# Kernel optimization log

Hardware: AMD Instinct MI355X
Metric: run time of the kernel (lower is better)

The kernel has to match this reference:

```python
import jax, jax.numpy as jnp
import numpy as np

T = 32            # timesteps_count
DT = 1e-3
TAU_MEM_INV = 100.0   # norse LIFParameters default (1/1e-2)
TAU_SYN_INV = 200.0   # norse default (1/5e-3)
V_TH = 1.0
ALPHA = 100.0         # SuperSpike surrogate slope


@jax.custom_vjp
def superspike(x):
    # Heaviside forward, SuperSpike surrogate backward (norse 'super' method)
    return (x > 0).astype(x.dtype)

def _ss_fwd(x):
    return (x > 0).astype(x.dtype), x

def _ss_bwd(x, g):
    return (g / (ALPHA * jnp.abs(x) + 1.0) ** 2,)

superspike.defvjp(_ss_fwd, _ss_bwd)


def setup_inputs() -> dict:
    key = jax.random.key(0)
    k1, k2 = jax.random.split(key)
    image = jax.random.uniform(k1, (4096, 1, 28, 28), dtype=jnp.float32)
    # LILinearCell input weights, shape [out_features, in_features]
    W = jax.random.normal(k2, (10, 784), dtype=jnp.float32) * np.sqrt(2.0 / 784.0).astype(np.float32)
    return {"image": image, "W": W}


def reference(image, W):
    B = image.shape[0]
    x = image.reshape(B, -1)  # [B, 784] constant input current

    def step(carry, _):
        v_enc, v0, i0, v_out, i_out = carry
        # --- ConstantCurrentLIFEncoder (lif_current_encoder step) ---
        v_enc = v_enc + DT * TAU_MEM_INV * (-v_enc + x)
        z_enc = superspike(v_enc - V_TH)
        v_enc = v_enc - z_enc * v_enc  # reset to v_reset = 0
        # --- LIFCell (feed-forward LIF step) ---
        v_dec = v0 + DT * TAU_MEM_INV * (-v0 + i0)
        i_dec = i0 - DT * TAU_SYN_INV * i0
        z0 = superspike(v_dec - V_TH)
        v0_new = (1.0 - z0) * v_dec          # v_reset = 0
        i0_new = i_dec + z_enc
        # --- LILinearCell (leaky integrator with linear input) ---
        i_jump = i_out + z0 @ W.T            # [B, 10]
        v_out_new = v_out + DT * TAU_MEM_INV * (-v_out + i_jump)
        i_out_new = i_jump - DT * TAU_SYN_INV * i_jump
        return (v_enc, v0_new, i0_new, v_out_new, i_out_new), v_out_new

    z784 = jnp.zeros_like(x)
    z10 = jnp.zeros((B, 10), dtype=x.dtype)
    _, vs = jax.lax.scan(step, (z784, z784, z784, z10, z10), None, length=T)
    v_max = jnp.max(vs, axis=0)              # max over timesteps, [B, 10]
    return jax.nn.log_softmax(v_max, axis=1)
```

## Files before the change

### kernel.cpp

```cpp
#include <hip/hip_runtime.h>
#include <math.h>


#define T_STEPS 32
#define N_IN 784
#define N_OUT 10
#define NK 4

__global__ __launch_bounds__(256) void snn_fused_kernel(
    const float* __restrict__ image,
    const float* __restrict__ W,
    float* __restrict__ out)
{
    constexpr float DT_TMI  = 0.1f;
    constexpr float DEC_SYN = 0.8f;
    constexpr float V_TH    = 1.0f;
    constexpr float NEG_LOG10 = -2.30258509299404568402f;

    const int b   = blockIdx.x;
    const int tid = threadIdx.x;
    const float* __restrict__ x_row = image + (size_t)b * N_IN;

    float xk[NK];
    int   jn[NK];
    int   can_spike = 0;
#pragma unroll
    for (int k = 0; k < NK; ++k) {
        int j = tid + 256 * k;
        jn[k] = j;
        xk[k] = (j < N_IN) ? x_row[j] : 0.0f;
        can_spike |= (xk[k] > V_TH);
    }

    if (!__syncthreads_or(can_spike)) {
        if (tid < N_OUT) out[(size_t)b * N_OUT + tid] = NEG_LOG10;
        return;
    }

    float v_enc[NK], v0[NK], i0[NK];
#pragma unroll
    for (int k = 0; k < NK; ++k) { v_enc[k] = 0.0f; v0[k] = 0.0f; i0[k] = 0.0f; }

    __shared__ float red[4][N_OUT];
    __shared__ float s_vout[N_OUT], s_iout[N_OUT], s_vmax[N_OUT];
    if (tid < N_OUT) {
        s_vout[tid] = 0.0f;
        s_iout[tid] = 0.0f;
        s_vmax[tid] = -INFINITY;
    }

    for (int t = 0; t < T_STEPS; ++t) {
        float s[N_OUT];
#pragma unroll
        for (int o = 0; o < N_OUT; ++o) s[o] = 0.0f;
        int any_spike = 0;

#pragma unroll
        for (int k = 0; k < NK; ++k) {
            v_enc[k] += DT_TMI * (xk[k] - v_enc[k]);
            float z_enc = (v_enc[k] > V_TH) ? 1.0f : 0.0f;
            v_enc[k] = (v_enc[k] > V_TH) ? 0.0f : v_enc[k];
            float v_dec = v0[k] + DT_TMI * (i0[k] - v0[k]);
            float i_dec = DEC_SYN * i0[k];
            bool  z0    = v_dec > V_TH;
            v0[k] = z0 ? 0.0f : v_dec;
            i0[k] = i_dec + z_enc;
            if (z0 && jn[k] < N_IN) {
                any_spike = 1;
#pragma unroll
                for (int o = 0; o < N_OUT; ++o)
                    s[o] += W[o * N_IN + jn[k]];
            }
        }

        const int any = __syncthreads_or(any_spike);

        if (any) {
#pragma unroll
            for (int o = 0; o < N_OUT; ++o) {
                float v = s[o];
                v += __shfl_down(v, 32, 64);
                v += __shfl_down(v, 16, 64);
                v += __shfl_down(v,  8, 64);
                v += __shfl_down(v,  4, 64);
                v += __shfl_down(v,  2, 64);
                v += __shfl_down(v,  1, 64);
                s[o] = v;
            }
            const int wave = tid >> 6;
            if ((tid & 63) == 0) {
#pragma unroll
                for (int o = 0; o < N_OUT; ++o) red[wave][o] = s[o];
            }
            __syncthreads();
        }

        if (tid < N_OUT) {
            float jump = s_iout[tid];
            if (any)
                jump += red[0][tid] + red[1][tid] + red[2][tid] + red[3][tid];
            float v = s_vout[tid] + DT_TMI * (jump - s_vout[tid]);
            s_vout[tid] = v;
            s_iout[tid] = DEC_SYN * jump;
            s_vmax[tid] = fmaxf(s_vmax[tid], v);
        }
    }

    __syncthreads();
    if (tid == 0) {
        float m = -INFINITY;
#pragma unroll
        for (int o = 0; o < N_OUT; ++o) m = fmaxf(m, s_vmax[o]);
        float sum = 0.0f;
#pragma unroll
        for (int o = 0; o < N_OUT; ++o) sum += expf(s_vmax[o] - m);
        const float lse = m + logf(sum);
        float* orow = out + (size_t)b * N_OUT;
#pragma unroll
        for (int o = 0; o < N_OUT; ++o) orow[o] = s_vmax[o] - lse;
    }
}

extern "C" void kernel_launch(void* const* d_in, const int* in_sizes, int n_in,
                              void* d_out, int out_size, void* d_ws, size_t ws_size,
                              hipStream_t stream) {
    const float* image = (const float*)d_in[0];
    const float* W     = (const float*)d_in[1];
    float*       out   = (float*)d_out;

    const int B = in_sizes[0] / N_IN;
    snn_fused_kernel<<<B, 256, 0, stream>>>(image, W, out);
}
```

Measured before the change: 62.43 us.

## Map one image row per wavefront and keep neuron state in global workspace

```diff
diff --git a/kernel.cpp b/kernel.cpp
--- a/kernel.cpp
+++ b/kernel.cpp
@@ -2,122 +2,137 @@
 #include <math.h>
 
 
+#define N_IN   784
+#define N_OUT  10
 #define T_STEPS 32
-#define N_IN 784
-#define N_OUT 10
-#define NK 4
+#define ROW_F4 196
+#define WS_ROW 2382
 
-__global__ __launch_bounds__(256) void snn_fused_kernel(
+__global__ __launch_bounds__(256) void snn_wave_kernel(
     const float* __restrict__ image,
     const float* __restrict__ W,
-    float* __restrict__ out)
+    float* __restrict__ out,
+    float* __restrict__ ws,
+    int B)
 {
     constexpr float DT_TMI  = 0.1f;
     constexpr float DEC_SYN = 0.8f;
     constexpr float V_TH    = 1.0f;
     constexpr float NEG_LOG10 = -2.30258509299404568402f;
 
-    const int b   = blockIdx.x;
-    const int tid = threadIdx.x;
-    const float* __restrict__ x_row = image + (size_t)b * N_IN;
+    const int wave = threadIdx.x >> 6;
+    const int lane = threadIdx.x & 63;
+    const int row  = blockIdx.x * 4 + wave;
+    if (row >= B) return;
 
-    float xk[NK];
-    int   jn[NK];
-    int   can_spike = 0;
-#pragma unroll
-    for (int k = 0; k < NK; ++k) {
-        int j = tid + 256 * k;
-        jn[k] = j;
-        xk[k] = (j < N_IN) ? x_row[j] : 0.0f;
-        can_spike |= (xk[k] > V_TH);
-    }
+    const float4* __restrict__ x4 = (const float4*)(image + (size_t)row * N_IN);
 
-    if (!__syncthreads_or(can_spike)) {
-        if (tid < N_OUT) out[(size_t)b * N_OUT + tid] = NEG_LOG10;
+    const bool has4 = (lane < 4);
+    float4 c0 = x4[lane];
+    float4 c1 = x4[lane + 64];
+    float4 c2 = x4[lane + 128];
+    float4 c3 = has4 ? x4[lane + 192] : make_float4(0.f, 0.f, 0.f, 0.f);
+
+    float m = fmaxf(fmaxf(fmaxf(c0.x, c0.y), fmaxf(c0.z, c0.w)),
+                    fmaxf(fmaxf(c1.x, c1.y), fmaxf(c1.z, c1.w)));
+    m = fmaxf(m, fmaxf(fmaxf(c2.x, c2.y), fmaxf(c2.z, c2.w)));
+    m = fmaxf(m, fmaxf(fmaxf(c3.x, c3.y), fmaxf(c3.z, c3.w)));
+
+    if (!__any(m > V_TH)) {
+        if (lane < N_OUT) out[(size_t)row * N_OUT + lane] = NEG_LOG10;
         return;
     }
 
-    float v_enc[NK], v0[NK], i0[NK];
+    float* const rb   = ws + (size_t)row * WS_ROW;
+    float* const p_ve = rb;
+    float* const p_v0 = rb + N_IN;
+    float* const p_i0 = rb + 2 * N_IN;
+    float* const p_ro = rb + 3 * N_IN;
+
+    const float xv[16] = { c0.x, c0.y, c0.z, c0.w,  c1.x, c1.y, c1.z, c1.w,
+                           c2.x, c2.y, c2.z, c2.w,  c3.x, c3.y, c3.z, c3.w };
+    const int   cbase[4] = { lane, lane + 64, lane + 128, lane + 192 };
+    const int   nch = has4 ? 4 : 3;
+
+    for (int c = 0; c < nch; ++c) {
+        const int j0 = 4 * cbase[c];
 #pragma unroll
-    for (int k = 0; k < NK; ++k) { v_enc[k] = 0.0f; v0[k] = 0.0f; i0[k] = 0.0f; }
-
-    __shared__ float red[4][N_OUT];
-    __shared__ float s_vout[N_OUT], s_iout[N_OUT], s_vmax[N_OUT];
-    if (tid < N_OUT) {
-        s_vout[tid] = 0.0f;
-        s_iout[tid] = 0.0f;
-        s_vmax[tid] = -INFINITY;
+        for (int e = 0; e < 4; ++e) {
+            p_ve[j0 + e] = 0.0f; p_v0[j0 + e] = 0.0f; p_i0[j0 + e] = 0.0f;
+        }
+    }
+    if (lane == 0) {
+#pragma unroll
+        for (int o = 0; o < N_OUT; ++o) {
+            p_ro[o] = 0.0f;
+            p_ro[10 + o] = 0.0f;
+            p_ro[20 + o] = -INFINITY;
+        }
     }
 
     for (int t = 0; t < T_STEPS; ++t) {
         float s[N_OUT];
 #pragma unroll
         for (int o = 0; o < N_OUT; ++o) s[o] = 0.0f;
-        int any_spike = 0;
 
+        for (int c = 0; c < nch; ++c) {
+            const int j0 = 4 * cbase[c];
 #pragma unroll
-        for (int k = 0; k < NK; ++k) {
-            v_enc[k] += DT_TMI * (xk[k] - v_enc[k]);
-            float z_enc = (v_enc[k] > V_TH) ? 1.0f : 0.0f;
-            v_enc[k] = (v_enc[k] > V_TH) ? 0.0f : v_enc[k];
-            float v_dec = v0[k] + DT_TMI * (i0[k] - v0[k]);
-            float i_dec = DEC_SYN * i0[k];
-            bool  z0    = v_dec > V_TH;
-            v0[k] = z0 ? 0.0f : v_dec;
-            i0[k] = i_dec + z_enc;
-            if (z0 && jn[k] < N_IN) {
-                any_spike = 1;
+            for (int e = 0; e < 4; ++e) {
+                const int j = j0 + e;
+                const float x = xv[4 * c + e];
+                float ve = p_ve[j], v0 = p_v0[j], i0 = p_i0[j];
+                ve += DT_TMI * (x - ve);
+                const float z_enc = (ve > V_TH) ? 1.0f : 0.0f;
+                ve = (ve > V_TH) ? 0.0f : ve;
+                const float v_dec = v0 + DT_TMI * (i0 - v0);
+                const float i_dec = DEC_SYN * i0;
+                const bool  z0    = v_dec > V_TH;
+                p_ve[j] = ve;
+                p_v0[j] = z0 ? 0.0f : v_dec;
+                p_i0[j] = i_dec + z_enc;
+                if (z0) {
 #pragma unroll
-                for (int o = 0; o < N_OUT; ++o)
-                    s[o] += W[o * N_IN + jn[k]];
+                    for (int o = 0; o < N_OUT; ++o) s[o] += W[o * N_IN + j];
+                }
             }
         }
 
-        const int any = __syncthreads_or(any_spike);
+#pragma unroll
+        for (int o = 0; o < N_OUT; ++o) {
+            float v = s[o];
+            v += __shfl_down(v, 32, 64);
+            v += __shfl_down(v, 16, 64);
+            v += __shfl_down(v,  8, 64);
+            v += __shfl_down(v,  4, 64);
+            v += __shfl_down(v,  2, 64);
+            v += __shfl_down(v,  1, 64);
+            s[o] = v;
+        }
 
-        if (any) {
+        if (lane == 0) {
 #pragma unroll
             for (int o = 0; o < N_OUT; ++o) {
-                float v = s[o];
-                v += __shfl_down(v, 32, 64);
-                v += __shfl_down(v, 16, 64);
-                v += __shfl_down(v,  8, 64);
-                v += __shfl_down(v,  4, 64);
-                v += __shfl_down(v,  2, 64);
-                v += __shfl_down(v,  1, 64);
-                s[o] = v;
+                const float jump = p_ro[10 + o] + s[o];
+                const float v    = p_ro[o] + DT_TMI * (jump - p_ro[o]);
+                p_ro[o]      = v;
+                p_ro[10 + o] = DEC_SYN * jump;
+                p_ro[20 + o] = fmaxf(p_ro[20 + o], v);
             }
-            const int wave = tid >> 6;
-            if ((tid & 63) == 0) {
-#pragma unroll
-                for (int o = 0; o < N_OUT; ++o) red[wave][o] = s[o];
-            }
-            __syncthreads();
-        }
-
-        if (tid < N_OUT) {
-            float jump = s_iout[tid];
-            if (any)
-                jump += red[0][tid] + red[1][tid] + red[2][tid] + red[3][tid];
-            float v = s_vout[tid] + DT_TMI * (jump - s_vout[tid]);
-            s_vout[tid] = v;
-            s_iout[tid] = DEC_SYN * jump;
-            s_vmax[tid] = fmaxf(s_vmax[tid], v);
         }
     }
 
-    __syncthreads();
-    if (tid == 0) {
-        float m = -INFINITY;
+    if (lane == 0) {
+        float mm = -INFINITY;
 #pragma unroll
-        for (int o = 0; o < N_OUT; ++o) m = fmaxf(m, s_vmax[o]);
+        for (int o = 0; o < N_OUT; ++o) mm = fmaxf(mm, p_ro[20 + o]);
         float sum = 0.0f;
 #pragma unroll
-        for (int o = 0; o < N_OUT; ++o) sum += expf(s_vmax[o] - m);
-        const float lse = m + logf(sum);
-        float* orow = out + (size_t)b * N_OUT;
+        for (int o = 0; o < N_OUT; ++o) sum += expf(p_ro[20 + o] - mm);
+        const float lse = mm + logf(sum);
+        float* orow = out + (size_t)row * N_OUT;
 #pragma unroll
-        for (int o = 0; o < N_OUT; ++o) orow[o] = s_vmax[o] - lse;
+        for (int o = 0; o < N_OUT; ++o) orow[o] = p_ro[20 + o] - lse;
     }
 }
 
@@ -129,5 +144,6 @@
     float*       out   = (float*)d_out;
 
     const int B = in_sizes[0] / N_IN;
-    snn_fused_kernel<<<B, 256, 0, stream>>>(image, W, out);
+    const int blocks = (B + 3) / 4;
+    snn_wave_kernel<<<blocks, 256, 0, stream>>>(image, W, out, (float*)d_ws, B);
 }
```

After: 61.09 us. -2.1%, faster.
